# Optimization experiments

Hardware: AMD Instinct MI355X
Metric: run time of the kernel (lower is better)

The kernel has to match this reference:

```python
import jax, jax.numpy as jnp
import numpy as np

B, L, T, D, F = 8, 12, 36, 1024, 3  # batch, local len, hist samples (n*tau), nodes, features
C = 32  # c_out


def setup_inputs() -> dict:
    key = jax.random.key(0)
    ks = jax.random.split(key, 8)
    s = 1.0 / np.sqrt(F)  # conv fan-in init scale
    return {
        "x_local": jax.random.normal(ks[0], (B, L, D, F), jnp.float32),
        "x_hist": jax.random.normal(ks[1], (B, L, T, D, F), jnp.float32),
        "Wq": jax.random.normal(ks[2], (C, F), jnp.float32) * s,
        "bq": jax.random.normal(ks[3], (C,), jnp.float32) * s,
        "Wm": jax.random.normal(ks[4], (C, F), jnp.float32) * s,
        "bm": jax.random.normal(ks[5], (C,), jnp.float32) * s,
        "Wc": jax.random.normal(ks[6], (C, F), jnp.float32) * s,
        "bc": jax.random.normal(ks[7], (C,), jnp.float32) * s,
    }


def reference(x_local, x_hist, Wq, bq, Wm, bm, Wc, bc):
    # 1x1 Conv2d/Conv3d over the feature channel F == pointwise linear in f.
    # torch permutes are absorbed into einsum axis ordering.
    q = jnp.einsum('bldf,cf->bcld', x_local, Wq) + bq[None, :, None, None]        # (B,C,L,D)
    m = jnp.einsum('bltdf,cf->bcltd', x_hist, Wm) + bm[None, :, None, None, None]  # (B,C,L,T,D)
    c = jnp.einsum('bltdf,cf->bcltd', x_hist, Wc) + bc[None, :, None, None, None]  # (B,C,L,T,D)
    mq = jnp.einsum('bcltd,bcld->bclt', m, q)                                     # scores (B,C,L,T)
    att = jax.nn.softmax(jax.nn.relu(mq), axis=-1)
    o = jnp.einsum('bclt,bcltd->bcld', att, c)                                    # memory read (B,C,L,D)
    return q + o
```

## Files before the change

kernel.cpp:

```cpp
#include <hip/hip_runtime.h>
#include <math.h>

#define BB 8
#define LL 12
#define TT 36
#define DD 1024
#define CC 32

__global__ __launch_bounds__(64) void k_Z(const float* __restrict__ xl,
                                          const float* __restrict__ xh,
                                          float* __restrict__ Zg,
                                          float* __restrict__ XLg) {
  const int blk  = blockIdx.x;
  const int bl   = blk / TT;
  const int lane = threadIdx.x;
  const float4* xh4 = (const float4*)xh + (size_t)blk * 768;
  const float4* xl4 = (const float4*)xl + (size_t)bl  * 768;

  float4 a4[12], b4[12];
  #pragma unroll
  for (int j = 0; j < 4; ++j)
    #pragma unroll
    for (int i = 0; i < 3; ++i)
      a4[j*3+i] = xh4[3*lane + 192*j + i];
  #pragma unroll
  for (int j = 0; j < 4; ++j)
    #pragma unroll
    for (int i = 0; i < 3; ++i)
      b4[j*3+i] = xl4[3*lane + 192*j + i];

  float Z00=0,Z01=0,Z02=0,Z10=0,Z11=0,Z12=0,Z20=0,Z21=0,Z22=0;
  float H0=0,H1=0,H2=0;
  const float* a = (const float*)a4;
  const float* b = (const float*)b4;
  #pragma unroll
  for (int k = 0; k < 16; ++k) {
    const float x0=a[k*3], x1=a[k*3+1], x2=a[k*3+2];
    const float y0=b[k*3], y1=b[k*3+1], y2=b[k*3+2];
    Z00 = fmaf(x0,y0,Z00); Z01 = fmaf(x0,y1,Z01); Z02 = fmaf(x0,y2,Z02);
    Z10 = fmaf(x1,y0,Z10); Z11 = fmaf(x1,y1,Z11); Z12 = fmaf(x1,y2,Z12);
    Z20 = fmaf(x2,y0,Z20); Z21 = fmaf(x2,y1,Z21); Z22 = fmaf(x2,y2,Z22);
    H0 += x0; H1 += x1; H2 += x2;
  }

  float v[12] = {Z00,Z01,Z02,Z10,Z11,Z12,Z20,Z21,Z22,H0,H1,H2};
  #pragma unroll
  for (int off = 32; off > 0; off >>= 1)
    #pragma unroll
    for (int j = 0; j < 12; ++j) v[j] += __shfl_down(v[j], off);

  if (lane == 0) {
    float4* o = (float4*)(Zg + (size_t)blk * 16);
    o[0] = make_float4(v[0], v[1], v[2],  v[3]);
    o[1] = make_float4(v[4], v[5], v[6],  v[7]);
    o[2] = make_float4(v[8], v[9], v[10], v[11]);
  }

  if (blk == bl * TT) {
    float s0=0.f, s1=0.f, s2=0.f;
    #pragma unroll
    for (int k = 0; k < 16; ++k) {
      s0 += b[k*3]; s1 += b[k*3+1]; s2 += b[k*3+2];
    }
    #pragma unroll
    for (int off = 32; off > 0; off >>= 1) {
      s0 += __shfl_down(s0, off);
      s1 += __shfl_down(s1, off);
      s2 += __shfl_down(s2, off);
    }
    if (lane == 0) {
      XLg[bl*4+0] = s0; XLg[bl*4+1] = s1; XLg[bl*4+2] = s2;
    }
  }
}

__global__ __launch_bounds__(256, 3) void k_out(const float* __restrict__ xl,
                                                const float* __restrict__ xh,
                                                const float* __restrict__ Zg,
                                                const float* __restrict__ XLg,
                                                const float* __restrict__ Wm,
                                                const float* __restrict__ bm,
                                                const float* __restrict__ Wq,
                                                const float* __restrict__ bq,
                                                const float* __restrict__ Wc,
                                                const float* __restrict__ bc,
                                                float* __restrict__ out) {
  __shared__ __align__(16) float ZS[TT * 16];
  __shared__ float S[TT][CC];
  __shared__ __align__(16) float PS[TT * 3 * CC];
  __shared__ float mxv[CC], inv[CC];
  const int bl = blockIdx.x;
  const int b = bl / LL, l = bl % LL;
  const int dh = blockIdx.y;
  const int tid = threadIdx.x;
  const int c = tid & 31;

  if (tid < TT * 4) ((float4*)ZS)[tid] = ((const float4*)(Zg + (size_t)bl * TT * 16))[tid];
  __syncthreads();

  {
    const float XL0 = XLg[bl*4+0], XL1 = XLg[bl*4+1], XL2 = XLg[bl*4+2];
    const float wm0 = Wm[c*3], wm1 = Wm[c*3+1], wm2 = Wm[c*3+2];
    const float wq0 = Wq[c*3], wq1 = Wq[c*3+1], wq2 = Wq[c*3+2];
    const float bqv = bq[c], bmv = bm[c];
    const float K = bmv * (fmaf(wq0, XL0, fmaf(wq1, XL1, wq2 * XL2)) + 1024.f * bqv);
    for (int idx = tid; idx < TT * CC; idx += 256) {
      const int t = idx >> 5;
      const float* z = &ZS[t * 16];
      float m = K;
      m = fmaf(wm0, fmaf(wq0, z[0], fmaf(wq1, z[1], fmaf(wq2, z[2], bqv * z[9]))),  m);
      m = fmaf(wm1, fmaf(wq0, z[3], fmaf(wq1, z[4], fmaf(wq2, z[5], bqv * z[10]))), m);
      m = fmaf(wm2, fmaf(wq0, z[6], fmaf(wq1, z[7], fmaf(wq2, z[8], bqv * z[11]))), m);
      S[t][c] = fmaxf(m, 0.f);
    }
  }
  __syncthreads();

  if (tid < CC) {
    float mx = 0.f;
    #pragma unroll
    for (int t = 0; t < TT; ++t) mx = fmaxf(mx, S[t][tid]);
    float ssum = 0.f;
    #pragma unroll
    for (int t = 0; t < TT; ++t) ssum += __expf(S[t][tid] - mx);
    mxv[tid] = mx;
    inv[tid] = 1.f / ssum;
  }
  __syncthreads();

  {
    const float wc0 = Wc[c*3], wc1 = Wc[c*3+1], wc2 = Wc[c*3+2];
    const float mxc = mxv[c], invc = inv[c];
    for (int idx = tid; idx < TT * CC; idx += 256) {
      const int t = idx >> 5;
      const float e = __expf(S[t][c] - mxc) * invc;
      PS[(t*3+0)*CC + c] = e * wc0;
      PS[(t*3+1)*CC + c] = e * wc1;
      PS[(t*3+2)*CC + c] = e * wc2;
    }
  }
  __syncthreads();

  const int g  = tid & 31;
  const int h5 = tid >> 5;
  const int c0 = h5 * 4;
  const int dg = dh * 32 + g;

  const float4* base = (const float4*)xh + (size_t)bl * TT * 768 + dg * 3;
  float4 buf[6][3];
  #pragma unroll
  for (int j = 0; j < 6; ++j)
    #pragma unroll
    for (int i = 0; i < 3; ++i) buf[j][i] = base[(size_t)j * 768 + i];

  float4 ql[3];
  {
    const float4* xl4 = (const float4*)xl + (size_t)bl * 768 + dg * 3;
    #pragma unroll
    for (int i = 0; i < 3; ++i) ql[i] = xl4[i];
  }

  float acc[4][4];
  #pragma unroll
  for (int u = 0; u < 4; ++u)
    #pragma unroll
    for (int dd = 0; dd < 4; ++dd) acc[u][dd] = 0.f;

  const float4* PS4 = (const float4*)PS;
  #pragma unroll
  for (int t = 0; t < TT; ++t) {
    const int sl = t % 6;
    float xv[12];
    {
      const float* x = (const float*)buf[sl];
      #pragma unroll
      for (int i = 0; i < 12; ++i) xv[i] = x[i];
    }
    if (t + 6 < TT) {
      const float4* p = base + (size_t)(t + 6) * 768;
      #pragma unroll
      for (int i = 0; i < 3; ++i) buf[sl][i] = p[i];
    }
    const float4 P0 = PS4[(t*3+0)*8 + h5];
    const float4 P1 = PS4[(t*3+1)*8 + h5];
    const float4 P2 = PS4[(t*3+2)*8 + h5];
    const float p0[4] = {P0.x, P0.y, P0.z, P0.w};
    const float p1[4] = {P1.x, P1.y, P1.z, P1.w};
    const float p2[4] = {P2.x, P2.y, P2.z, P2.w};
    #pragma unroll
    for (int u = 0; u < 4; ++u)
      #pragma unroll
      for (int dd = 0; dd < 4; ++dd)
        acc[u][dd] = fmaf(p0[u], xv[dd*3],
                     fmaf(p1[u], xv[dd*3+1],
                     fmaf(p2[u], xv[dd*3+2], acc[u][dd])));
  }

  const float* y = (const float*)ql;
  #pragma unroll
  for (int u = 0; u < 4; ++u) {
    const int cc = c0 + u;
    const float w0 = Wq[cc*3], w1 = Wq[cc*3+1], w2 = Wq[cc*3+2];
    const float b0 = bq[cc], bcv = bc[cc];
    float4 o;
    o.x = acc[u][0] + bcv + fmaf(w0, y[0], fmaf(w1, y[1],  fmaf(w2, y[2],  b0)));
    o.y = acc[u][1] + bcv + fmaf(w0, y[3], fmaf(w1, y[4],  fmaf(w2, y[5],  b0)));
    o.z = acc[u][2] + bcv + fmaf(w0, y[6], fmaf(w1, y[7],  fmaf(w2, y[8],  b0)));
    o.w = acc[u][3] + bcv + fmaf(w0, y[9], fmaf(w1, y[10], fmaf(w2, y[11], b0)));
    *(float4*)(out + (((size_t)b * CC + cc) * LL + l) * DD + dg * 4) = o;
  }
}

extern "C" void kernel_launch(void* const* d_in, const int* in_sizes, int n_in,
                              void* d_out, int out_size, void* d_ws, size_t ws_size,
                              hipStream_t stream) {
  const float* xl = (const float*)d_in[0];
  const float* xh = (const float*)d_in[1];
  const float* Wq = (const float*)d_in[2];
  const float* bq = (const float*)d_in[3];
  const float* Wm = (const float*)d_in[4];
  const float* bm = (const float*)d_in[5];
  const float* Wc = (const float*)d_in[6];
  const float* bc = (const float*)d_in[7];
  float* out = (float*)d_out;

  float* Zg  = (float*)d_ws;
  float* XLg = Zg + (size_t)BB * LL * TT * 16;

  k_Z  <<<dim3(BB * LL * TT), 64,  0, stream>>>(xl, xh, Zg, XLg);
  k_out<<<dim3(BB * LL, 8),   256, 0, stream>>>(xl, xh, Zg, XLg, Wm, bm, Wq, bq,
                                                Wc, bc, out);
}
```

Before: 115.5 us.

## Fuse score-reduction kernel into output kernel, recomputing Z per block

Merges the two kernels into one. Each block now computes the per-timestep cross-products Z and the sum XL for its (b,l) slice itself, keeping them in shared memory instead of writing them to a global workspace and launching a second kernel. This removes one launch and the global round trip for Z. The cost is that all 8 D-chunk blocks of the same (b,l) redo the full-D reduction over x_hist, so x_hist is read about eight times more, relying on cache hits, and each wave runs a serial 9-timestep loop before the main phase.

```diff
diff --git a/kernel.cpp b/kernel.cpp
--- a/kernel.cpp
+++ b/kernel.cpp
@@ -7,99 +7,98 @@
 #define DD 1024
 #define CC 32
 
-__global__ __launch_bounds__(64) void k_Z(const float* __restrict__ xl,
-                                          const float* __restrict__ xh,
-                                          float* __restrict__ Zg,
-                                          float* __restrict__ XLg) {
-  const int blk  = blockIdx.x;
-  const int bl   = blk / TT;
-  const int lane = threadIdx.x;
-  const float4* xh4 = (const float4*)xh + (size_t)blk * 768;
-  const float4* xl4 = (const float4*)xl + (size_t)bl  * 768;
-
-  float4 a4[12], b4[12];
-  #pragma unroll
-  for (int j = 0; j < 4; ++j)
-    #pragma unroll
-    for (int i = 0; i < 3; ++i)
-      a4[j*3+i] = xh4[3*lane + 192*j + i];
-  #pragma unroll
-  for (int j = 0; j < 4; ++j)
-    #pragma unroll
-    for (int i = 0; i < 3; ++i)
-      b4[j*3+i] = xl4[3*lane + 192*j + i];
-
-  float Z00=0,Z01=0,Z02=0,Z10=0,Z11=0,Z12=0,Z20=0,Z21=0,Z22=0;
-  float H0=0,H1=0,H2=0;
-  const float* a = (const float*)a4;
-  const float* b = (const float*)b4;
-  #pragma unroll
-  for (int k = 0; k < 16; ++k) {
-    const float x0=a[k*3], x1=a[k*3+1], x2=a[k*3+2];
-    const float y0=b[k*3], y1=b[k*3+1], y2=b[k*3+2];
-    Z00 = fmaf(x0,y0,Z00); Z01 = fmaf(x0,y1,Z01); Z02 = fmaf(x0,y2,Z02);
-    Z10 = fmaf(x1,y0,Z10); Z11 = fmaf(x1,y1,Z11); Z12 = fmaf(x1,y2,Z12);
-    Z20 = fmaf(x2,y0,Z20); Z21 = fmaf(x2,y1,Z21); Z22 = fmaf(x2,y2,Z22);
-    H0 += x0; H1 += x1; H2 += x2;
-  }
-
-  float v[12] = {Z00,Z01,Z02,Z10,Z11,Z12,Z20,Z21,Z22,H0,H1,H2};
-  #pragma unroll
-  for (int off = 32; off > 0; off >>= 1)
-    #pragma unroll
-    for (int j = 0; j < 12; ++j) v[j] += __shfl_down(v[j], off);
-
-  if (lane == 0) {
-    float4* o = (float4*)(Zg + (size_t)blk * 16);
-    o[0] = make_float4(v[0], v[1], v[2],  v[3]);
-    o[1] = make_float4(v[4], v[5], v[6],  v[7]);
-    o[2] = make_float4(v[8], v[9], v[10], v[11]);
-  }
-
-  if (blk == bl * TT) {
-    float s0=0.f, s1=0.f, s2=0.f;
-    #pragma unroll
-    for (int k = 0; k < 16; ++k) {
-      s0 += b[k*3]; s1 += b[k*3+1]; s2 += b[k*3+2];
-    }
-    #pragma unroll
-    for (int off = 32; off > 0; off >>= 1) {
-      s0 += __shfl_down(s0, off);
-      s1 += __shfl_down(s1, off);
-      s2 += __shfl_down(s2, off);
-    }
-    if (lane == 0) {
-      XLg[bl*4+0] = s0; XLg[bl*4+1] = s1; XLg[bl*4+2] = s2;
-    }
-  }
-}
-
-__global__ __launch_bounds__(256, 3) void k_out(const float* __restrict__ xl,
-                                                const float* __restrict__ xh,
-                                                const float* __restrict__ Zg,
-                                                const float* __restrict__ XLg,
-                                                const float* __restrict__ Wm,
-                                                const float* __restrict__ bm,
-                                                const float* __restrict__ Wq,
-                                                const float* __restrict__ bq,
-                                                const float* __restrict__ Wc,
-                                                const float* __restrict__ bc,
-                                                float* __restrict__ out) {
+__global__ __launch_bounds__(256, 3) void k_fused(
+    const float* __restrict__ xl, const float* __restrict__ xh,
+    const float* __restrict__ Wm, const float* __restrict__ bm,
+    const float* __restrict__ Wq, const float* __restrict__ bq,
+    const float* __restrict__ Wc, const float* __restrict__ bc,
+    float* __restrict__ out) {
   __shared__ __align__(16) float ZS[TT * 16];
   __shared__ float S[TT][CC];
   __shared__ __align__(16) float PS[TT * 3 * CC];
   __shared__ float mxv[CC], inv[CC];
-  const int bl = blockIdx.x;
-  const int b = bl / LL, l = bl % LL;
-  const int dh = blockIdx.y;
-  const int tid = threadIdx.x;
-  const int c = tid & 31;
-
-  if (tid < TT * 4) ((float4*)ZS)[tid] = ((const float4*)(Zg + (size_t)bl * TT * 16))[tid];
-  __syncthreads();
-
-  {
-    const float XL0 = XLg[bl*4+0], XL1 = XLg[bl*4+1], XL2 = XLg[bl*4+2];
+  __shared__ float XLs[4];
+
+  const int tid  = threadIdx.x;
+  const int lane = tid & 63;
+  const int wid  = tid >> 6;
+  const int bl   = blockIdx.x % 96;
+  const int dh   = blockIdx.x / 96;
+
+  {
+    const float4* xl4 = (const float4*)xl + (size_t)bl * 768;
+    float4 b4[12];
+    #pragma unroll
+    for (int j = 0; j < 4; ++j)
+      #pragma unroll
+      for (int i = 0; i < 3; ++i)
+        b4[j*3+i] = xl4[3*lane + 192*j + i];
+    const float* b = (const float*)b4;
+
+    for (int k = 0; k < 9; ++k) {
+      const int t   = wid * 9 + k;
+      const float4* xh4 = (const float4*)xh + ((size_t)bl * TT + t) * 768;
+
+      float4 a4[12];
+      #pragma unroll
+      for (int j = 0; j < 4; ++j)
+        #pragma unroll
+        for (int i = 0; i < 3; ++i)
+          a4[j*3+i] = xh4[3*lane + 192*j + i];
+
+      float Z00=0,Z01=0,Z02=0,Z10=0,Z11=0,Z12=0,Z20=0,Z21=0,Z22=0;
+      float H0=0,H1=0,H2=0;
+      const float* a = (const float*)a4;
+      #pragma unroll
+      for (int q = 0; q < 16; ++q) {
+        const float x0=a[q*3], x1=a[q*3+1], x2=a[q*3+2];
+        const float y0=b[q*3], y1=b[q*3+1], y2=b[q*3+2];
+        Z00 = fmaf(x0,y0,Z00); Z01 = fmaf(x0,y1,Z01); Z02 = fmaf(x0,y2,Z02);
+        Z10 = fmaf(x1,y0,Z10); Z11 = fmaf(x1,y1,Z11); Z12 = fmaf(x1,y2,Z12);
+        Z20 = fmaf(x2,y0,Z20); Z21 = fmaf(x2,y1,Z21); Z22 = fmaf(x2,y2,Z22);
+        H0 += x0; H1 += x1; H2 += x2;
+      }
+
+      float v[12] = {Z00,Z01,Z02,Z10,Z11,Z12,Z20,Z21,Z22,H0,H1,H2};
+      #pragma unroll
+      for (int off = 32; off > 0; off >>= 1)
+        #pragma unroll
+        for (int j = 0; j < 12; ++j) v[j] += __shfl_down(v[j], off);
+
+      if (lane == 0) {
+        float4* o = (float4*)&ZS[t * 16];
+        o[0] = make_float4(v[0], v[1], v[2],  v[3]);
+        o[1] = make_float4(v[4], v[5], v[6],  v[7]);
+        o[2] = make_float4(v[8], v[9], v[10], v[11]);
+      }
+    }
+
+    if (wid == 0) {
+      float s0=0.f, s1=0.f, s2=0.f;
+      #pragma unroll
+      for (int q = 0; q < 16; ++q) {
+        s0 += b[q*3]; s1 += b[q*3+1]; s2 += b[q*3+2];
+      }
+      #pragma unroll
+      for (int off = 32; off > 0; off >>= 1) {
+        s0 += __shfl_down(s0, off);
+        s1 += __shfl_down(s1, off);
+        s2 += __shfl_down(s2, off);
+      }
+      if (lane == 0) { XLs[0] = s0; XLs[1] = s1; XLs[2] = s2; }
+    }
+  }
+  __syncthreads();
+
+  const int b  = bl / LL, l = bl % LL;
+  const int c  = tid & 31;
+  const int g  = tid & 31;
+  const int h5 = tid >> 5;
+  const int c0 = h5 * 4;
+  const int dg = dh * 32 + g;
+
+  {
+    const float XL0 = XLs[0], XL1 = XLs[1], XL2 = XLs[2];
     const float wm0 = Wm[c*3], wm1 = Wm[c*3+1], wm2 = Wm[c*3+2];
     const float wq0 = Wq[c*3], wq1 = Wq[c*3+1], wq2 = Wq[c*3+2];
     const float bqv = bq[c], bmv = bm[c];
@@ -141,11 +140,6 @@
   }
   __syncthreads();
 
-  const int g  = tid & 31;
-  const int h5 = tid >> 5;
-  const int c0 = h5 * 4;
-  const int dg = dh * 32 + g;
-
   const float4* base = (const float4*)xh + (size_t)bl * TT * 768 + dg * 3;
   float4 buf[6][3];
   #pragma unroll
@@ -223,11 +217,8 @@
   const float* Wc = (const float*)d_in[6];
   const float* bc = (const float*)d_in[7];
   float* out = (float*)d_out;
-
-  float* Zg  = (float*)d_ws;
-  float* XLg = Zg + (size_t)BB * LL * TT * 16;
-
-  k_Z  <<<dim3(BB * LL * TT), 64,  0, stream>>>(xl, xh, Zg, XLg);
-  k_out<<<dim3(BB * LL, 8),   256, 0, stream>>>(xl, xh, Zg, XLg, Wm, bm, Wq, bq,
-                                                Wc, bc, out);
+  (void)d_ws; (void)ws_size;
+
+  k_fused<<<dim3(BB * LL * 8), dim3(256), 0, stream>>>(
+      xl, xh, Wm, bm, Wq, bq, Wc, bc, out);
 }
```

Result: slower. 133.9 us (+16.0%).
